# Performance work log

Hardware: AMD Instinct MI355X
Metric: run time of the kernel (lower is better)

Reference implementation:

```python
import jax, jax.numpy as jnp
import numpy as np
import math

B, T, D, H, P, NPASS = 2, 2048, 1024, 16, 256, 3


def setup_inputs() -> dict:
    key = jax.random.key(0)
    ks = jax.random.split(key, 8)
    x = jax.random.normal(ks[0], (B, T, D), jnp.float32)
    scale_gamma = 1.0 + 0.1 * jax.random.normal(ks[1], (D,), jnp.float32)
    scale_beta = 0.1 * jax.random.normal(ks[2], (D,), jnp.float32)
    qkv_w = 0.02 * jax.random.normal(ks[3], (3 * D, D), jnp.float32)
    o_w = 0.02 * jax.random.normal(ks[4], (D, D), jnp.float32)
    norm1_w = jnp.ones((D,), jnp.float32)
    norm2_w = jnp.ones((D,), jnp.float32)
    angles = 0.1 * jax.random.normal(ks[5], (NPASS, P), jnp.float32)
    gate = jnp.ones((NPASS, D), jnp.float32)
    bias = jnp.zeros((NPASS, D), jnp.float32)
    # seeded random permutations matching torch.manual_seed(42+p*1000); torch.randperm
    pis, pjs = [], []
    for p in range(NPASS):
        rng = np.random.RandomState(42 + p * 1000)
        perm = rng.permutation(D)
        pis.append(perm[:P])
        pjs.append(perm[P:2 * P])
    pi = jnp.asarray(np.stack(pis), jnp.int32)
    pj = jnp.asarray(np.stack(pjs), jnp.int32)
    return dict(x=x, scale_gamma=scale_gamma, scale_beta=scale_beta, qkv_w=qkv_w,
                o_w=o_w, norm1_w=norm1_w, norm2_w=norm2_w, angles=angles,
                gate=gate, bias=bias, pi=pi, pj=pj)


def _rmsnorm(x, w):
    eps = jnp.finfo(x.dtype).eps
    return x * jax.lax.rsqrt(jnp.mean(x * x, axis=-1, keepdims=True) + eps) * w


def reference(x, scale_gamma, scale_beta, qkv_w, o_w, norm1_w, norm2_w,
              angles, gate, bias, pi, pj):
    Bs, Ts, Ds = x.shape
    hd = Ds // H
    # --- attention branch ---
    h = _rmsnorm(x, norm1_w) * scale_gamma + scale_beta
    qkv = (h @ qkv_w.T).reshape(Bs, Ts, 3, H, hd)
    qkv = jnp.moveaxis(qkv, 2, 0)            # [3, B, T, H, hd]
    q, k, v = (jnp.swapaxes(qkv[i], 1, 2) for i in range(3))  # [B, H, T, hd]
    scores = jnp.einsum('bhqd,bhkd->bhqk', q, k) / math.sqrt(hd)
    causal = jnp.tril(jnp.ones((Ts, Ts), bool))
    scores = jnp.where(causal, scores, -jnp.inf)
    attn = jax.nn.softmax(scores, axis=-1)
    out = jnp.einsum('bhqk,bhkd->bhqd', attn, v)
    out = jnp.swapaxes(out, 1, 2).reshape(Bs, Ts, Ds)
    x = x + out @ o_w.T
    # --- rotation pseudo-FFN branch ---
    h = _rmsnorm(x, norm2_w) * scale_gamma + scale_beta
    r = h
    for p in range(NPASS):
        cos_a = jnp.cos(angles[p])
        sin_a = jnp.sin(angles[p])
        hi = r[..., pi[p]]
        hj = r[..., pj[p]]
        r = r.at[..., pi[p]].set(hi * cos_a - hj * sin_a)
        r = r.at[..., pj[p]].set(hi * sin_a + hj * cos_a)
        r = jax.nn.silu(r * gate[p] + bias[p])
    return x + r - h
```

## Files before the change

kernel.cpp:

```cpp
#include <hip/hip_runtime.h>
#include <hip/hip_bf16.h>

#define B_ 2
#define T_ 2048
#define D_ 1024
#define H_ 16
#define HD_ 64
#define NP_ 3
#define P_ 256

#define SCALE2 0.18033688011112042f

typedef short bf16x8 __attribute__((ext_vector_type(8)));
typedef float f32x4 __attribute__((ext_vector_type(4)));

__device__ __forceinline__ float bf2f(__hip_bfloat16 v) { return __bfloat162float(v); }
__device__ __forceinline__ __hip_bfloat16 f2bf(float v) { return __float2bfloat16(v); }

__device__ __forceinline__ unsigned pack2bf(float a, float b) {
    union { __hip_bfloat16 h; unsigned short u; } ua, ub;
    ua.h = f2bf(a); ub.h = f2bf(b);
    return (unsigned)ua.u | ((unsigned)ub.u << 16);
}

#define GLOAD_LDS16(gp, lp) \
    __builtin_amdgcn_global_load_lds( \
        (const __attribute__((address_space(1))) void*)(gp), \
        (__attribute__((address_space(3))) void*)(lp), 16, 0, 0)

__global__ __launch_bounds__(256) void detect_kernel(
    const unsigned short* __restrict__ xs, int* __restrict__ flag)
{
    __shared__ int cnt;
    if (threadIdx.x == 0) cnt = 0;
    __syncthreads();
    int bad = 0;
    for (int i = threadIdx.x; i < 16384; i += 256) {
        int e = (xs[i] >> 7) & 0xFF;
        if (e >= 0xB8) bad++;
    }
    if (bad) atomicAdd(&cnt, bad);
    __syncthreads();
    if (threadIdx.x == 0) *flag = (cnt >= 8) ? 1 : 0;
}

__global__ __launch_bounds__(256) void cvt16_2_kernel(
    const void* __restrict__ a, const void* __restrict__ bsrc,
    __hip_bfloat16* __restrict__ da, __hip_bfloat16* __restrict__ db,
    int na, int ntot, const int* __restrict__ flag)
{
    int i = blockIdx.x * 256 + threadIdx.x;
    if (i >= ntot) return;
    int f = *flag;
    if (i < na)
        da[i] = f ? f2bf(((const float*)a)[i]) : ((const __hip_bfloat16*)a)[i];
    else {
        int k = i - na;
        db[k] = f ? f2bf(((const float*)bsrc)[k]) : ((const __hip_bfloat16*)bsrc)[k];
    }
}

__global__ __launch_bounds__(256) void cvt_small_kernel(
    const void* __restrict__ g,  const void* __restrict__ b,
    const void* __restrict__ n1, const void* __restrict__ n2,
    const void* __restrict__ ang, const void* __restrict__ gt,
    const void* __restrict__ bi,
    float* __restrict__ dst, const int* __restrict__ flag)
{
    int i = blockIdx.x * 256 + threadIdx.x;
    if (i >= 11008) return;
    const void* src; int off;
    if      (i < 1024) { src = g;   off = i; }
    else if (i < 2048) { src = b;   off = i - 1024; }
    else if (i < 3072) { src = n1;  off = i - 2048; }
    else if (i < 4096) { src = n2;  off = i - 3072; }
    else if (i < 4864) { src = ang; off = i - 4096; }
    else if (i < 7936) { src = gt;  off = i - 4864; }
    else               { src = bi;  off = i - 7936; }
    dst[i] = (*flag) ? ((const float*)src)[off]
                     : bf2f(((const __hip_bfloat16*)src)[off]);
}

__global__ __launch_bounds__(256) void rmsnorm1_kernel(
    const void* __restrict__ xraw,
    const float* __restrict__ gamma,
    const float* __restrict__ beta,
    const float* __restrict__ w,
    const int* __restrict__ flag,
    __hip_bfloat16* __restrict__ out,
    float* __restrict__ xcopy)
{
    int row = blockIdx.x;
    int t = threadIdx.x;
    int f = *flag;
    float eps = f ? 1.1920929e-7f : 0.0078125f;
    float v[4];
    if (f) {
        const float4 xv = ((const float4*)((const float*)xraw + (size_t)row * D_))[t];
        v[0] = xv.x; v[1] = xv.y; v[2] = xv.z; v[3] = xv.w;
    } else {
        const __hip_bfloat16* xr = (const __hip_bfloat16*)xraw + (size_t)row * D_;
#pragma unroll
        for (int c = 0; c < 4; c++) v[c] = bf2f(xr[t * 4 + c]);
    }
    float ss = 0.f;
#pragma unroll
    for (int c = 0; c < 4; c++) ss += v[c] * v[c];
#pragma unroll
    for (int m = 32; m; m >>= 1) ss += __shfl_xor(ss, m, 64);
    __shared__ float red[4];
    int wv = t >> 6;
    if ((t & 63) == 0) red[wv] = ss;
    __syncthreads();
    float scale = rsqrtf((red[0] + red[1] + red[2] + red[3]) * (1.0f / D_) + eps);
#pragma unroll
    for (int c = 0; c < 4; c++) {
        int e = t * 4 + c;
        size_t idx = (size_t)row * D_ + e;
        xcopy[idx] = v[c];
        out[idx] = f2bf(v[c] * scale * w[e] * gamma[e] + beta[e]);
    }
}

__global__ __launch_bounds__(256) void gemm_bt_bf16_kernel(
    const __hip_bfloat16* __restrict__ A,
    const __hip_bfloat16* __restrict__ Bm,
    __hip_bfloat16* __restrict__ C,
    int M, int N, int K, int nscale, float qscale)
{
    __shared__ __attribute__((aligned(16))) __hip_bfloat16 As[128 * 32];
    __shared__ __attribute__((aligned(16))) __hip_bfloat16 Bs[128 * 32];
    int tid = threadIdx.x;
    int bm = blockIdx.y, bn = blockIdx.x;
    int lane = tid & 63, wv = tid >> 6;
    int wm = wv >> 1, wn = wv & 1;
    int q = lane >> 4, mr = lane & 15;

    f32x4 acc[4][4] = {};

    for (int k0 = 0; k0 < K; k0 += 32) {
#pragma unroll
        for (int s = 0; s < 2; s++) {
            int e = (s * 256 + tid) * 8;
            int r = e >> 5, c = e & 31;
            GLOAD_LDS16(&A[(size_t)(bm * 128 + r) * K + k0 + c], &As[e]);
            GLOAD_LDS16(&Bm[(size_t)(bn * 128 + r) * K + k0 + c], &Bs[e]);
        }
        __syncthreads();
        bf16x8 af[4], bfr[4];
#pragma unroll
        for (int i = 0; i < 4; i++)
            af[i] = *(const bf16x8*)(&As[(wm * 64 + i * 16 + mr) * 32 + q * 8]);
#pragma unroll
        for (int j = 0; j < 4; j++)
            bfr[j] = *(const bf16x8*)(&Bs[(wn * 64 + j * 16 + mr) * 32 + q * 8]);
#pragma unroll
        for (int i = 0; i < 4; i++)
#pragma unroll
            for (int j = 0; j < 4; j++)
                acc[i][j] = __builtin_amdgcn_mfma_f32_16x16x32_bf16(af[i], bfr[j], acc[i][j], 0, 0, 0);
        __syncthreads();
    }

#pragma unroll
    for (int i = 0; i < 4; i++)
#pragma unroll
        for (int r = 0; r < 4; r++) {
            int m = bm * 128 + wm * 64 + i * 16 + q * 4 + r;
#pragma unroll
            for (int j = 0; j < 4; j++) {
                int n = bn * 128 + wn * 64 + j * 16 + mr;
                float vv = acc[i][j][r];
                if (n < nscale) vv *= qscale;
                C[(size_t)m * N + n] = f2bf(vv);
            }
        }
}

__global__ __launch_bounds__(256) void gemm_bt_resid_kernel(
    const __hip_bfloat16* __restrict__ A,
    const __hip_bfloat16* __restrict__ Bm,
    const float* __restrict__ resid,
    float* __restrict__ C,
    int M, int N, int K)
{
    __shared__ __attribute__((aligned(16))) __hip_bfloat16 As[128 * 32];
    __shared__ __attribute__((aligned(16))) __hip_bfloat16 Bs[128 * 32];
    int tid = threadIdx.x;
    int bm = blockIdx.y, bn = blockIdx.x;
    int lane = tid & 63, wv = tid >> 6;
    int wm = wv >> 1, wn = wv & 1;
    int q = lane >> 4, mr = lane & 15;

    f32x4 acc[4][4] = {};

    for (int k0 = 0; k0 < K; k0 += 32) {
#pragma unroll
        for (int s = 0; s < 2; s++) {
            int e = (s * 256 + tid) * 8;
            int r = e >> 5, c = e & 31;
            GLOAD_LDS16(&A[(size_t)(bm * 128 + r) * K + k0 + c], &As[e]);
            GLOAD_LDS16(&Bm[(size_t)(bn * 128 + r) * K + k0 + c], &Bs[e]);
        }
        __syncthreads();
        bf16x8 af[4], bfr[4];
#pragma unroll
        for (int i = 0; i < 4; i++)
            af[i] = *(const bf16x8*)(&As[(wm * 64 + i * 16 + mr) * 32 + q * 8]);
#pragma unroll
        for (int j = 0; j < 4; j++)
            bfr[j] = *(const bf16x8*)(&Bs[(wn * 64 + j * 16 + mr) * 32 + q * 8]);
#pragma unroll
        for (int i = 0; i < 4; i++)
#pragma unroll
            for (int j = 0; j < 4; j++)
                acc[i][j] = __builtin_amdgcn_mfma_f32_16x16x32_bf16(af[i], bfr[j], acc[i][j], 0, 0, 0);
        __syncthreads();
    }

#pragma unroll
    for (int i = 0; i < 4; i++)
#pragma unroll
        for (int r = 0; r < 4; r++) {
            int m = bm * 128 + wm * 64 + i * 16 + q * 4 + r;
#pragma unroll
            for (int j = 0; j < 4; j++) {
                int n = bn * 128 + wn * 64 + j * 16 + mr;
                size_t idx = (size_t)m * N + n;
                C[idx] = resid[idx] + acc[i][j][r];
            }
        }
}

__global__ __launch_bounds__(256, 4) void attn_kernel(
    const __hip_bfloat16* __restrict__ qkv,
    __hip_bfloat16* __restrict__ attn_out)
{
    __shared__ __attribute__((aligned(16))) __hip_bfloat16 Ks[2][64 * 64];
    __shared__ __attribute__((aligned(16))) __hip_bfloat16 Vts[2][64 * 64];
    __shared__ __attribute__((aligned(16))) unsigned int Pd[4 * 512];

    int z = blockIdx.x;
    int qt0 = 31 - z, qt1 = z;
    int bh = blockIdx.y;
    int b = bh >> 4, h = bh & 15;
    int tid = threadIdx.x, lane = tid & 63, wv = tid >> 6;
    int q = lane >> 4, mr = lane & 15;
    int m8 = mr & 7;

    const size_t rs3 = 3 * D_;
    const __hip_bfloat16* qp = qkv + (size_t)(b * T_) * rs3 + h * HD_;
    const __hip_bfloat16* kp = qp + D_;
    const __hip_bfloat16* vp = qp + 2 * D_;

    int sr = tid >> 2;
    int sc = (tid & 3) * 16;
    int lc0 = sc >> 3;
    int swk = sr & 7;
    int kk_ = (tid & 31) * 2;
    int dd = (tid >> 5) * 8;
    int vlc = kk_ >> 3, voff = kk_ & 7;

    bf16x8 aq0, aq1, aqn0, aqn1;
    {
        const __hip_bfloat16* qrow = qp + (size_t)(qt0 * 64 + wv * 16 + mr) * rs3;
        aq0 = *(const bf16x8*)(qrow + q * 8);
        aq1 = *(const bf16x8*)(qrow + 32 + q * 8);
    }

    bf16x8 kr0 = *(const bf16x8*)(kp + (size_t)sr * rs3 + sc);
    bf16x8 kr1 = *(const bf16x8*)(kp + (size_t)sr * rs3 + sc + 8);
    bf16x8 vr0 = *(const bf16x8*)(vp + (size_t)kk_ * rs3 + dd);
    bf16x8 vr1 = *(const bf16x8*)(vp + (size_t)(kk_ + 1) * rs3 + dd);
    *(bf16x8*)(&Ks[0][sr * 64 + ((lc0 ^ swk) * 8)]) = kr0;
    *(bf16x8*)(&Ks[0][sr * 64 + (((lc0 + 1) ^ swk) * 8)]) = kr1;
    {
        unsigned int* vd = (unsigned int*)&Vts[0][0];
#pragma unroll
        for (int i = 0; i < 8; i++) {
            unsigned int wd = ((unsigned int)(unsigned short)vr0[i]) |
                              (((unsigned int)(unsigned short)vr1[i]) << 16);
            vd[((dd + i) * 64 + ((vlc ^ i) * 8 + voff)) >> 1] = wd;
        }
    }
    __syncthreads();

    float m_run = -INFINITY, l_run = 0.f;
    f32x4 o_acc[4] = {};
    unsigned int* Pw = &Pd[wv * 512];
    int qloc = wv * 16 + mr;

    for (int s = 0; s <= 32; s++) {
        int seg1 = (s > qt0);
        int kt = seg1 ? (s - qt0 - 1) : s;
        int qt = seg1 ? qt1 : qt0;
        int buf = s & 1;

        if (s < 32) {
            int ktn = (s + 1 > qt0) ? (s - qt0) : (s + 1);
            kr0 = *(const bf16x8*)(kp + (size_t)(ktn * 64 + sr) * rs3 + sc);
            kr1 = *(const bf16x8*)(kp + (size_t)(ktn * 64 + sr) * rs3 + sc + 8);
            vr0 = *(const bf16x8*)(vp + (size_t)(ktn * 64 + kk_) * rs3 + dd);
            vr1 = *(const bf16x8*)(vp + (size_t)(ktn * 64 + kk_ + 1) * rs3 + dd);
        }
        if (s == qt0) {
            const __hip_bfloat16* qrow = qp + (size_t)(qt1 * 64 + wv * 16 + mr) * rs3;
            aqn0 = *(const bf16x8*)(qrow + q * 8);
            aqn1 = *(const bf16x8*)(qrow + 32 + q * 8);
        }

        f32x4 sv[4] = {};
        {
            const __hip_bfloat16* Kb = &Ks[buf][0];
#pragma unroll
            for (int jn = 0; jn < 4; jn++)
                sv[jn] = __builtin_amdgcn_mfma_f32_16x16x32_bf16(
                    *(const bf16x8*)(&Kb[(jn * 16 + mr) * 64 + ((q ^ m8) * 8)]),
                    aq0, sv[jn], 0, 0, 0);
#pragma unroll
            for (int jn = 0; jn < 4; jn++)
                sv[jn] = __builtin_amdgcn_mfma_f32_16x16x32_bf16(
                    *(const bf16x8*)(&Kb[(jn * 16 + mr) * 64 + (((4 + q) ^ m8) * 8)]),
                    aq1, sv[jn], 0, 0, 0);
        }

        if (kt == qt) {
#pragma unroll
            for (int jn = 0; jn < 4; jn++)
#pragma unroll
                for (int r = 0; r < 4; r++)
                    if (jn * 16 + q * 4 + r > qloc) sv[jn][r] = -1e30f;
        }

        float mx = fmaxf(fmaxf(sv[0][0], sv[0][1]), fmaxf(sv[0][2], sv[0][3]));
#pragma unroll
        for (int jn = 1; jn < 4; jn++)
            mx = fmaxf(mx, fmaxf(fmaxf(sv[jn][0], sv[jn][1]), fmaxf(sv[jn][2], sv[jn][3])));
        mx = fmaxf(mx, __shfl_xor(mx, 16, 64));
        mx = fmaxf(mx, __shfl_xor(mx, 32, 64));
        float mn = fmaxf(m_run, mx);
        float alpha = exp2f(m_run - mn);
        m_run = mn;
        float psum = 0.f;
#pragma unroll
        for (int jn = 0; jn < 4; jn++)
#pragma unroll
            for (int r = 0; r < 4; r++) {
                float p = exp2f(sv[jn][r] - mn);
                sv[jn][r] = p;
                psum += p;
            }
        psum += __shfl_xor(psum, 16, 64);
        psum += __shfl_xor(psum, 32, 64);
        l_run = l_run * alpha + psum;
#pragma unroll
        for (int dt = 0; dt < 4; dt++)
#pragma unroll
            for (int r = 0; r < 4; r++)
                o_acc[dt][r] *= alpha;

#pragma unroll
        for (int jn = 0; jn < 4; jn++) {
            uint2 val;
            val.x = pack2bf(sv[jn][0], sv[jn][1]);
            val.y = pack2bf(sv[jn][2], sv[jn][3]);
            int dw4 = 2 * jn + (q >> 1);
            *(uint2*)(&Pw[mr * 32 + ((dw4 ^ m8) << 2) + 2 * (q & 1)]) = val;
        }

#pragma unroll
        for (int kk = 0; kk < 2; kk++) {
            bf16x8 bp = *(const bf16x8*)(&Pw[mr * 32 + (((4 * kk + q) ^ m8) << 2)]);
#pragma unroll
            for (int dt = 0; dt < 4; dt++) {
                bf16x8 bv = *(const bf16x8*)(&Vts[buf][(dt * 16 + mr) * 64 + (((kk * 4 + q) ^ m8) * 8)]);
                o_acc[dt] = __builtin_amdgcn_mfma_f32_16x16x32_bf16(bv, bp, o_acc[dt], 0, 0, 0);
            }
        }

        if (s < 32) {
            *(bf16x8*)(&Ks[buf ^ 1][sr * 64 + ((lc0 ^ swk) * 8)]) = kr0;
            *(bf16x8*)(&Ks[buf ^ 1][sr * 64 + (((lc0 + 1) ^ swk) * 8)]) = kr1;
            unsigned int* vd = (unsigned int*)&Vts[buf ^ 1][0];
#pragma unroll
            for (int i = 0; i < 8; i++) {
                unsigned int wd = ((unsigned int)(unsigned short)vr0[i]) |
                                  (((unsigned int)(unsigned short)vr1[i]) << 16);
                vd[((dd + i) * 64 + ((vlc ^ i) * 8 + voff)) >> 1] = wd;
            }
        }
        __syncthreads();

        if (s == qt0) {
            float inv = 1.0f / l_run;
            int trow = qt0 * 64 + wv * 16 + mr;
            __hip_bfloat16* op = attn_out + (size_t)(b * T_ + trow) * D_ + h * HD_;
#pragma unroll
            for (int dt = 0; dt < 4; dt++) {
                uint2 val;
                val.x = pack2bf(o_acc[dt][0] * inv, o_acc[dt][1] * inv);
                val.y = pack2bf(o_acc[dt][2] * inv, o_acc[dt][3] * inv);
                *(uint2*)(op + dt * 16 + q * 4) = val;
            }
            m_run = -INFINITY; l_run = 0.f;
#pragma unroll
            for (int dt = 0; dt < 4; dt++) o_acc[dt] = (f32x4){0.f, 0.f, 0.f, 0.f};
            aq0 = aqn0; aq1 = aqn1;
        }
    }

    {
        float inv = 1.0f / l_run;
        int trow = qt1 * 64 + wv * 16 + mr;
        __hip_bfloat16* op = attn_out + (size_t)(b * T_ + trow) * D_ + h * HD_;
#pragma unroll
        for (int dt = 0; dt < 4; dt++) {
            uint2 val;
            val.x = pack2bf(o_acc[dt][0] * inv, o_acc[dt][1] * inv);
            val.y = pack2bf(o_acc[dt][2] * inv, o_acc[dt][3] * inv);
            *(uint2*)(op + dt * 16 + q * 4) = val;
        }
    }
}

__global__ __launch_bounds__(256) void final_kernel(
    const float* __restrict__ xn,
    const float* __restrict__ gamma,
    const float* __restrict__ beta,
    const float* __restrict__ w2,
    const float* __restrict__ angles,
    const float* __restrict__ gate,
    const float* __restrict__ bias,
    const int* __restrict__ pi,
    const int* __restrict__ pj,
    const int* __restrict__ flag,
    void* __restrict__ outp)
{
    __shared__ float rbuf[D_];
    __shared__ float red[4];
    int row = blockIdx.x, t = threadIdx.x;
    int f = *flag;
    float eps = f ? 1.1920929e-7f : 0.0078125f;
    const float* xr = xn + (size_t)row * D_;
    float x4[4];
    float ss = 0.f;
#pragma unroll
    for (int c = 0; c < 4; c++) { x4[c] = xr[t * 4 + c]; ss += x4[c] * x4[c]; }
#pragma unroll
    for (int m = 32; m; m >>= 1) ss += __shfl_xor(ss, m, 64);
    int wv = t >> 6;
    if ((t & 63) == 0) red[wv] = ss;
    __syncthreads();
    float scale = rsqrtf((red[0] + red[1] + red[2] + red[3]) * (1.0f / D_) + eps);
    float hloc[4];
#pragma unroll
    for (int c = 0; c < 4; c++) {
        int e = t * 4 + c;
        float hv = x4[c] * scale * w2[e] * gamma[e] + beta[e];
        hloc[c] = hv;
        rbuf[e] = hv;
    }
    __syncthreads();
    for (int p = 0; p < NP_; p++) {
        float a = angles[p * P_ + t];
        float ca = __cosf(a), sa = __sinf(a);
        int ip = pi[p * P_ + t], jp = pj[p * P_ + t];
        float hi = rbuf[ip], hj = rbuf[jp];
        rbuf[ip] = hi * ca - hj * sa;
        rbuf[jp] = hi * sa + hj * ca;
        __syncthreads();
#pragma unroll
        for (int c = 0; c < 4; c++) {
            int e = t * 4 + c;
            float v = rbuf[e] * gate[p * D_ + e] + bias[p * D_ + e];
            rbuf[e] = v / (1.f + __expf(-v));
        }
        __syncthreads();
    }
#pragma unroll
    for (int c = 0; c < 4; c++) {
        int e = t * 4 + c;
        float ov = x4[c] + rbuf[e] - hloc[c];
        size_t idx = (size_t)row * D_ + e;
        if (f) ((float*)outp)[idx] = ov;
        else   ((__hip_bfloat16*)outp)[idx] = f2bf(ov);
    }
}

extern "C" void kernel_launch(void* const* d_in, const int* in_sizes, int n_in,
                              void* d_out, int out_size, void* d_ws, size_t ws_size,
                              hipStream_t stream)
{
    const void* x      = d_in[0];
    const void* gamma  = d_in[1];
    const void* beta   = d_in[2];
    const void* qkv_w  = d_in[3];
    const void* o_w    = d_in[4];
    const void* n1w    = d_in[5];
    const void* n2w    = d_in[6];
    const void* angles = d_in[7];
    const void* gate   = d_in[8];
    const void* bias   = d_in[9];
    const int* pi = (const int*)d_in[10];
    const int* pj = (const int*)d_in[11];

    const int M = B_ * T_;
    char* ws = (char*)d_ws;
    const size_t MB = 1u << 20;
    int*   flag   = (int*)ws;
    float* smalls = (float*)(ws + 4096);
    float* gf   = smalls;
    float* bf   = smalls + 1024;
    float* n1f  = smalls + 2048;
    float* n2f  = smalls + 3072;
    float* angf = smalls + 4096;
    float* gtf  = smalls + 4864;
    float* bif  = smalls + 7936;
    float*          xf32 = (float*)         (ws +  1 * MB);
    __hip_bfloat16* wbf  = (__hip_bfloat16*)(ws + 17 * MB);
    __hip_bfloat16* owbf = (__hip_bfloat16*)(ws + 23 * MB);
    __hip_bfloat16* h1   = (__hip_bfloat16*)(ws + 25 * MB);
    __hip_bfloat16* qkv  = (__hip_bfloat16*)(ws + 33 * MB);
    float*          xnew = (float*)         (ws + 33 * MB);

    detect_kernel<<<1, 256, 0, stream>>>((const unsigned short*)x, flag);

    cvt_small_kernel<<<43, 256, 0, stream>>>(gamma, beta, n1w, n2w, angles, gate, bias,
                                             smalls, flag);
    cvt16_2_kernel<<<(4 * D_ * D_ + 255) / 256, 256, 0, stream>>>(
        qkv_w, o_w, wbf, owbf, 3 * D_ * D_, 4 * D_ * D_, flag);

    rmsnorm1_kernel<<<M, 256, 0, stream>>>(x, gf, bf, n1f, flag, h1, xf32);

    gemm_bt_bf16_kernel<<<dim3(3 * D_ / 128, M / 128), 256, 0, stream>>>(
        h1, wbf, qkv, M, 3 * D_, D_, D_, SCALE2);

    attn_kernel<<<dim3(16, B_ * H_), 256, 0, stream>>>(qkv, h1);

    gemm_bt_resid_kernel<<<dim3(D_ / 128, M / 128), 256, 0, stream>>>(
        h1, owbf, xf32, xnew, M, D_, D_);

    final_kernel<<<M, 256, 0, stream>>>(xnew, gf, bf, n2f, angf, gtf, bif,
                                        pi, pj, flag, d_out);
}
```

Baseline: 251.7 us.

## Split attention KV loop across two wave groups with split-K softmax merge

The attention kernel grows from 256 to 512 threads. Two groups of four waves each process alternating KV tiles from a 4-deep shared-memory ring buffer, and the two partial online-softmax states (max, sum, accumulator) are merged through shared memory at the end. This halves the serial KV-loop length per block to add parallelism on a grid of only 512 blocks. The cost is double the LDS footprint, a merge step with extra syncs, and lower occupancy per CU.

```diff
diff --git a/kernel.cpp b/kernel.cpp
--- a/kernel.cpp
+++ b/kernel.cpp
@@ -232,50 +232,50 @@
         }
 }
 
-__global__ __launch_bounds__(256, 4) void attn_kernel(
+__global__ __launch_bounds__(512, 4) void attn_kernel(
     const __hip_bfloat16* __restrict__ qkv,
     __hip_bfloat16* __restrict__ attn_out)
 {
-    __shared__ __attribute__((aligned(16))) __hip_bfloat16 Ks[2][64 * 64];
-    __shared__ __attribute__((aligned(16))) __hip_bfloat16 Vts[2][64 * 64];
-    __shared__ __attribute__((aligned(16))) unsigned int Pd[4 * 512];
+    __shared__ __attribute__((aligned(16))) __hip_bfloat16 Ks[4][64 * 64];
+    __shared__ __attribute__((aligned(16))) __hip_bfloat16 Vts[4][64 * 64];
+    __shared__ __attribute__((aligned(16))) unsigned int Pd[8 * 512];
 
     int z = blockIdx.x;
     int qt0 = 31 - z, qt1 = z;
+    int n0 = qt0 + 1;
     int bh = blockIdx.y;
     int b = bh >> 4, h = bh & 15;
     int tid = threadIdx.x, lane = tid & 63, wv = tid >> 6;
-    int q = lane >> 4, mr = lane & 15;
-    int m8 = mr & 7;
+    int g = wv >> 2, qw = wv & 3;
+    int q = lane >> 4, mr = lane & 15, m8 = mr & 7;
 
     const size_t rs3 = 3 * D_;
     const __hip_bfloat16* qp = qkv + (size_t)(b * T_) * rs3 + h * HD_;
     const __hip_bfloat16* kp = qp + D_;
     const __hip_bfloat16* vp = qp + 2 * D_;
 
-    int sr = tid >> 2;
-    int sc = (tid & 3) * 16;
-    int lc0 = sc >> 3;
-    int swk = sr & 7;
-    int kk_ = (tid & 31) * 2;
-    int dd = (tid >> 5) * 8;
-    int vlc = kk_ >> 3, voff = kk_ & 7;
-
-    bf16x8 aq0, aq1, aqn0, aqn1;
+    int tl = tid >> 8;
+    int t8 = tid & 255;
+    int sr = t8 >> 2, sc = (t8 & 3) * 16, lc0 = sc >> 3, swk = sr & 7;
+    int kk_ = (t8 & 31) * 2, dd = (t8 >> 5) * 8, vlc = kk_ >> 3, voff = kk_ & 7;
+
+    bf16x8 aq0, aq1;
     {
-        const __hip_bfloat16* qrow = qp + (size_t)(qt0 * 64 + wv * 16 + mr) * rs3;
+        const __hip_bfloat16* qrow = qp + (size_t)(qt0 * 64 + qw * 16 + mr) * rs3;
         aq0 = *(const bf16x8*)(qrow + q * 8);
         aq1 = *(const bf16x8*)(qrow + 32 + q * 8);
     }
 
-    bf16x8 kr0 = *(const bf16x8*)(kp + (size_t)sr * rs3 + sc);
-    bf16x8 kr1 = *(const bf16x8*)(kp + (size_t)sr * rs3 + sc + 8);
-    bf16x8 vr0 = *(const bf16x8*)(vp + (size_t)kk_ * rs3 + dd);
-    bf16x8 vr1 = *(const bf16x8*)(vp + (size_t)(kk_ + 1) * rs3 + dd);
-    *(bf16x8*)(&Ks[0][sr * 64 + ((lc0 ^ swk) * 8)]) = kr0;
-    *(bf16x8*)(&Ks[0][sr * 64 + (((lc0 + 1) ^ swk) * 8)]) = kr1;
+    bf16x8 kr0, kr1, vr0, vr1;
     {
-        unsigned int* vd = (unsigned int*)&Vts[0][0];
+        const __hip_bfloat16* ksrc = kp + (size_t)(tl * 64 + sr) * rs3 + sc;
+        kr0 = *(const bf16x8*)(ksrc);
+        kr1 = *(const bf16x8*)(ksrc + 8);
+        vr0 = *(const bf16x8*)(vp + (size_t)(tl * 64 + kk_) * rs3 + dd);
+        vr1 = *(const bf16x8*)(vp + (size_t)(tl * 64 + kk_ + 1) * rs3 + dd);
+        *(bf16x8*)(&Ks[tl][sr * 64 + ((lc0 ^ swk) * 8)]) = kr0;
+        *(bf16x8*)(&Ks[tl][sr * 64 + (((lc0 + 1) ^ swk) * 8)]) = kr1;
+        unsigned int* vd = (unsigned int*)&Vts[tl][0];
 #pragma unroll
         for (int i = 0; i < 8; i++) {
             unsigned int wd = ((unsigned int)(unsigned short)vr0[i]) |
@@ -287,101 +287,119 @@
 
     float m_run = -INFINITY, l_run = 0.f;
     f32x4 o_acc[4] = {};
+    float pm = -INFINITY, pl = 0.f;
+    f32x4 p_acc[4] = {};
+    int curSeg = 0;
     unsigned int* Pw = &Pd[wv * 512];
-    int qloc = wv * 16 + mr;
-
-    for (int s = 0; s <= 32; s++) {
-        int seg1 = (s > qt0);
-        int kt = seg1 ? (s - qt0 - 1) : s;
-        int qt = seg1 ? qt1 : qt0;
-        int buf = s & 1;
-
-        if (s < 32) {
-            int ktn = (s + 1 > qt0) ? (s - qt0) : (s + 1);
-            kr0 = *(const bf16x8*)(kp + (size_t)(ktn * 64 + sr) * rs3 + sc);
-            kr1 = *(const bf16x8*)(kp + (size_t)(ktn * 64 + sr) * rs3 + sc + 8);
-            vr0 = *(const bf16x8*)(vp + (size_t)(ktn * 64 + kk_) * rs3 + dd);
-            vr1 = *(const bf16x8*)(vp + (size_t)(ktn * 64 + kk_ + 1) * rs3 + dd);
-        }
-        if (s == qt0) {
-            const __hip_bfloat16* qrow = qp + (size_t)(qt1 * 64 + wv * 16 + mr) * rs3;
-            aqn0 = *(const bf16x8*)(qrow + q * 8);
-            aqn1 = *(const bf16x8*)(qrow + 32 + q * 8);
-        }
-
-        f32x4 sv[4] = {};
-        {
-            const __hip_bfloat16* Kb = &Ks[buf][0];
+    int qloc = qw * 16 + mr;
+
+    for (int u = 0; u < 17; u++) {
+        int f = 2 * u + g;
+        int fpre = 2 * u + 2 + tl;
+
+        if (fpre <= 32) {
+            int ktp = (fpre < n0) ? fpre : fpre - n0;
+            const __hip_bfloat16* ksrc = kp + (size_t)(ktp * 64 + sr) * rs3 + sc;
+            kr0 = *(const bf16x8*)(ksrc);
+            kr1 = *(const bf16x8*)(ksrc + 8);
+            vr0 = *(const bf16x8*)(vp + (size_t)(ktp * 64 + kk_) * rs3 + dd);
+            vr1 = *(const bf16x8*)(vp + (size_t)(ktp * 64 + kk_ + 1) * rs3 + dd);
+        }
+
+        if (f <= 32) {
+            int seg = (f >= n0);
+            if (seg != curSeg) {
+                pm = m_run; pl = l_run;
+#pragma unroll
+                for (int dt = 0; dt < 4; dt++) {
+                    p_acc[dt] = o_acc[dt];
+                    o_acc[dt] = (f32x4){0.f, 0.f, 0.f, 0.f};
+                }
+                m_run = -INFINITY; l_run = 0.f;
+                const __hip_bfloat16* qrow = qp + (size_t)(qt1 * 64 + qw * 16 + mr) * rs3;
+                aq0 = *(const bf16x8*)(qrow + q * 8);
+                aq1 = *(const bf16x8*)(qrow + 32 + q * 8);
+                curSeg = 1;
+            }
+            int qt = seg ? qt1 : qt0;
+            int kt = seg ? f - n0 : f;
+            int buf = f & 3;
+
+            f32x4 sv[4] = {};
+            {
+                const __hip_bfloat16* Kb = &Ks[buf][0];
+#pragma unroll
+                for (int jn = 0; jn < 4; jn++)
+                    sv[jn] = __builtin_amdgcn_mfma_f32_16x16x32_bf16(
+                        *(const bf16x8*)(&Kb[(jn * 16 + mr) * 64 + ((q ^ m8) * 8)]),
+                        aq0, sv[jn], 0, 0, 0);
+#pragma unroll
+                for (int jn = 0; jn < 4; jn++)
+                    sv[jn] = __builtin_amdgcn_mfma_f32_16x16x32_bf16(
+                        *(const bf16x8*)(&Kb[(jn * 16 + mr) * 64 + (((4 + q) ^ m8) * 8)]),
+                        aq1, sv[jn], 0, 0, 0);
+            }
+
+            if (kt == qt) {
+#pragma unroll
+                for (int jn = 0; jn < 4; jn++)
+#pragma unroll
+                    for (int r = 0; r < 4; r++)
+                        if (jn * 16 + q * 4 + r > qloc) sv[jn][r] = -1e30f;
+            }
+
+            float mx = fmaxf(fmaxf(sv[0][0], sv[0][1]), fmaxf(sv[0][2], sv[0][3]));
+#pragma unroll
+            for (int jn = 1; jn < 4; jn++)
+                mx = fmaxf(mx, fmaxf(fmaxf(sv[jn][0], sv[jn][1]), fmaxf(sv[jn][2], sv[jn][3])));
+            mx = fmaxf(mx, __shfl_xor(mx, 16, 64));
+            mx = fmaxf(mx, __shfl_xor(mx, 32, 64));
+            float mn = fmaxf(m_run, mx);
+            float alpha = exp2f(m_run - mn);
+            m_run = mn;
+            float psum = 0.f;
 #pragma unroll
             for (int jn = 0; jn < 4; jn++)
-                sv[jn] = __builtin_amdgcn_mfma_f32_16x16x32_bf16(
-                    *(const bf16x8*)(&Kb[(jn * 16 + mr) * 64 + ((q ^ m8) * 8)]),
-                    aq0, sv[jn], 0, 0, 0);
-#pragma unroll
-            for (int jn = 0; jn < 4; jn++)
-                sv[jn] = __builtin_amdgcn_mfma_f32_16x16x32_bf16(
-                    *(const bf16x8*)(&Kb[(jn * 16 + mr) * 64 + (((4 + q) ^ m8) * 8)]),
-                    aq1, sv[jn], 0, 0, 0);
-        }
-
-        if (kt == qt) {
-#pragma unroll
-            for (int jn = 0; jn < 4; jn++)
+#pragma unroll
+                for (int r = 0; r < 4; r++) {
+                    float p = exp2f(sv[jn][r] - mn);
+                    sv[jn][r] = p;
+                    psum += p;
+                }
+            psum += __shfl_xor(psum, 16, 64);
+            psum += __shfl_xor(psum, 32, 64);
+            l_run = l_run * alpha + psum;
+#pragma unroll
+            for (int dt = 0; dt < 4; dt++)
 #pragma unroll
                 for (int r = 0; r < 4; r++)
-                    if (jn * 16 + q * 4 + r > qloc) sv[jn][r] = -1e30f;
-        }
-
-        float mx = fmaxf(fmaxf(sv[0][0], sv[0][1]), fmaxf(sv[0][2], sv[0][3]));
-#pragma unroll
-        for (int jn = 1; jn < 4; jn++)
-            mx = fmaxf(mx, fmaxf(fmaxf(sv[jn][0], sv[jn][1]), fmaxf(sv[jn][2], sv[jn][3])));
-        mx = fmaxf(mx, __shfl_xor(mx, 16, 64));
-        mx = fmaxf(mx, __shfl_xor(mx, 32, 64));
-        float mn = fmaxf(m_run, mx);
-        float alpha = exp2f(m_run - mn);
-        m_run = mn;
-        float psum = 0.f;
-#pragma unroll
-        for (int jn = 0; jn < 4; jn++)
-#pragma unroll
-            for (int r = 0; r < 4; r++) {
-                float p = exp2f(sv[jn][r] - mn);
-                sv[jn][r] = p;
-                psum += p;
-            }
-        psum += __shfl_xor(psum, 16, 64);
-        psum += __shfl_xor(psum, 32, 64);
-        l_run = l_run * alpha + psum;
-#pragma unroll
-        for (int dt = 0; dt < 4; dt++)
-#pragma unroll
-            for (int r = 0; r < 4; r++)
-                o_acc[dt][r] *= alpha;
-
-#pragma unroll
-        for (int jn = 0; jn < 4; jn++) {
-            uint2 val;
-            val.x = pack2bf(sv[jn][0], sv[jn][1]);
-            val.y = pack2bf(sv[jn][2], sv[jn][3]);
-            int dw4 = 2 * jn + (q >> 1);
-            *(uint2*)(&Pw[mr * 32 + ((dw4 ^ m8) << 2) + 2 * (q & 1)]) = val;
-        }
-
-#pragma unroll
-        for (int kk = 0; kk < 2; kk++) {
-            bf16x8 bp = *(const bf16x8*)(&Pw[mr * 32 + (((4 * kk + q) ^ m8) << 2)]);
-#pragma unroll
-            for (int dt = 0; dt < 4; dt++) {
-                bf16x8 bv = *(const bf16x8*)(&Vts[buf][(dt * 16 + mr) * 64 + (((kk * 4 + q) ^ m8) * 8)]);
-                o_acc[dt] = __builtin_amdgcn_mfma_f32_16x16x32_bf16(bv, bp, o_acc[dt], 0, 0, 0);
-            }
-        }
-
-        if (s < 32) {
-            *(bf16x8*)(&Ks[buf ^ 1][sr * 64 + ((lc0 ^ swk) * 8)]) = kr0;
-            *(bf16x8*)(&Ks[buf ^ 1][sr * 64 + (((lc0 + 1) ^ swk) * 8)]) = kr1;
-            unsigned int* vd = (unsigned int*)&Vts[buf ^ 1][0];
+                    o_acc[dt][r] *= alpha;
+
+#pragma unroll
+            for (int jn = 0; jn < 4; jn++) {
+                uint2 val;
+                val.x = pack2bf(sv[jn][0], sv[jn][1]);
+                val.y = pack2bf(sv[jn][2], sv[jn][3]);
+                int dw4 = 2 * jn + (q >> 1);
+                *(uint2*)(&Pw[mr * 32 + ((dw4 ^ m8) << 2) + 2 * (q & 1)]) = val;
+            }
+
+#pragma unroll
+            for (int kk = 0; kk < 2; kk++) {
+                bf16x8 bp = *(const bf16x8*)(&Pw[mr * 32 + (((4 * kk + q) ^ m8) << 2)]);
+#pragma unroll
+                for (int dt = 0; dt < 4; dt++) {
+                    bf16x8 bv = *(const bf16x8*)(&Vts[buf][(dt * 16 + mr) * 64 + (((kk * 4 + q) ^ m8) * 8)]);
+                    o_acc[dt] = __builtin_amdgcn_mfma_f32_16x16x32_bf16(bv, bp, o_acc[dt], 0, 0, 0);
+                }
+            }
+        }
+
+        if (fpre <= 32) {
+            int bufp = fpre & 3;
+            *(bf16x8*)(&Ks[bufp][sr * 64 + ((lc0 ^ swk) * 8)]) = kr0;
+            *(bf16x8*)(&Ks[bufp][sr * 64 + (((lc0 + 1) ^ swk) * 8)]) = kr1;
+            unsigned int* vd = (unsigned int*)&Vts[bufp][0];
 #pragma unroll
             for (int i = 0; i < 8; i++) {
                 unsigned int wd = ((unsigned int)(unsigned short)vr0[i]) |
@@ -390,36 +408,63 @@
             }
         }
         __syncthreads();
-
-        if (s == qt0) {
-            float inv = 1.0f / l_run;
-            int trow = qt0 * 64 + wv * 16 + mr;
+    }
+
+    if (curSeg == 0) {
+        pm = m_run; pl = l_run;
+#pragma unroll
+        for (int dt = 0; dt < 4; dt++) {
+            p_acc[dt] = o_acc[dt];
+            o_acc[dt] = (f32x4){0.f, 0.f, 0.f, 0.f};
+        }
+        m_run = -INFINITY; l_run = 0.f;
+    }
+
+    float* mO  = (float*)&Ks[0][0];
+    float* mML = (float*)&Vts[0][0];
+#pragma unroll
+    for (int segI = 0; segI < 2; segI++) {
+        float sm, sl; f32x4 so[4];
+        if (segI == 0) {
+            sm = pm; sl = pl;
+#pragma unroll
+            for (int dt = 0; dt < 4; dt++) so[dt] = p_acc[dt];
+        } else {
+            sm = m_run; sl = l_run;
+#pragma unroll
+            for (int dt = 0; dt < 4; dt++) so[dt] = o_acc[dt];
+        }
+        int slot = qw * 64 + lane;
+        if (g == 1) {
+            mML[slot * 2] = sm; mML[slot * 2 + 1] = sl;
+#pragma unroll
+            for (int dt = 0; dt < 4; dt++)
+#pragma unroll
+                for (int r = 0; r < 4; r++)
+                    mO[(dt * 4 + r) * 256 + slot] = so[dt][r];
+        }
+        __syncthreads();
+        if (g == 0) {
+            float m1 = mML[slot * 2], l1 = mML[slot * 2 + 1];
+            float mm = fmaxf(sm, m1);
+            float w0 = exp2f(sm - mm), w1 = exp2f(m1 - mm);
+            float inv = 1.0f / (sl * w0 + l1 * w1);
+            int qt = segI ? qt1 : qt0;
+            int trow = qt * 64 + qw * 16 + mr;
             __hip_bfloat16* op = attn_out + (size_t)(b * T_ + trow) * D_ + h * HD_;
 #pragma unroll
             for (int dt = 0; dt < 4; dt++) {
+                float v0 = (so[dt][0] * w0 + mO[(dt * 4 + 0) * 256 + slot] * w1) * inv;
+                float v1 = (so[dt][1] * w0 + mO[(dt * 4 + 1) * 256 + slot] * w1) * inv;
+                float v2 = (so[dt][2] * w0 + mO[(dt * 4 + 2) * 256 + slot] * w1) * inv;
+                float v3 = (so[dt][3] * w0 + mO[(dt * 4 + 3) * 256 + slot] * w1) * inv;
                 uint2 val;
-                val.x = pack2bf(o_acc[dt][0] * inv, o_acc[dt][1] * inv);
-                val.y = pack2bf(o_acc[dt][2] * inv, o_acc[dt][3] * inv);
+                val.x = pack2bf(v0, v1);
+                val.y = pack2bf(v2, v3);
                 *(uint2*)(op + dt * 16 + q * 4) = val;
             }
-            m_run = -INFINITY; l_run = 0.f;
-#pragma unroll
-            for (int dt = 0; dt < 4; dt++) o_acc[dt] = (f32x4){0.f, 0.f, 0.f, 0.f};
-            aq0 = aqn0; aq1 = aqn1;
-        }
-    }
-
-    {
-        float inv = 1.0f / l_run;
-        int trow = qt1 * 64 + wv * 16 + mr;
-        __hip_bfloat16* op = attn_out + (size_t)(b * T_ + trow) * D_ + h * HD_;
-#pragma unroll
-        for (int dt = 0; dt < 4; dt++) {
-            uint2 val;
-            val.x = pack2bf(o_acc[dt][0] * inv, o_acc[dt][1] * inv);
-            val.y = pack2bf(o_acc[dt][2] * inv, o_acc[dt][3] * inv);
-            *(uint2*)(op + dt * 16 + q * 4) = val;
-        }
+        }
+        __syncthreads();
     }
 }
 
@@ -535,7 +580,7 @@
     gemm_bt_bf16_kernel<<<dim3(3 * D_ / 128, M / 128), 256, 0, stream>>>(
         h1, wbf, qkv, M, 3 * D_, D_, D_, SCALE2);
 
-    attn_kernel<<<dim3(16, B_ * H_), 256, 0, stream>>>(qkv, h1);
+    attn_kernel<<<dim3(16, B_ * H_), 512, 0, stream>>>(qkv, h1);
 
     gemm_bt_resid_kernel<<<dim3(D_ / 128, M / 128), 256, 0, stream>>>(
         h1, owbf, xf32, xnew, M, D_, D_);
```

Measured after the change: 276.0 us. +9.6%, slower.
